# Kernel tuning notes

Measured on AMD Instinct MI355X. Metric: run time of the kernel, lower is better.

## Reference

```python
import jax, jax.numpy as jnp
import numpy as np

N, E, F, H, L, G = 100000, 1600000, 32, 128, 4, 64


def gru_cell(m, h, w_ih, b_ih, w_hh, b_hh):
    # torch.nn.GRUCell math; gate order: r, z, n
    gi = m @ w_ih.T + b_ih          # [N, 3H]
    gh = h @ w_hh.T + b_hh          # [N, 3H]
    i_r, i_z, i_n = jnp.split(gi, 3, axis=-1)
    h_r, h_z, h_n = jnp.split(gh, 3, axis=-1)
    r = jax.nn.sigmoid(i_r + h_r)
    z = jax.nn.sigmoid(i_z + h_z)
    n = jnp.tanh(i_n + r * h_n)
    return (1.0 - z) * n + z * h


def setup_inputs() -> dict:
    key = jax.random.key(0)
    ks = jax.random.split(key, 12)
    s = 0.05
    return {
        "x": jax.random.normal(ks[0], (N, F), jnp.float32),
        "edge_index": jax.random.randint(ks[1], (2, E), 0, N, jnp.int64),
        "batch": jnp.sort(jax.random.randint(ks[2], (N,), 0, G, jnp.int64)),
        "num_graphs": G,
        "W0": jax.random.normal(ks[3], (H, F), jnp.float32) * s,
        "conv_w": jax.random.normal(ks[4], (L, H, H), jnp.float32) * s,
        "w_ih": jax.random.normal(ks[5], (3 * H, H), jnp.float32) * s,
        "b_ih": jax.random.normal(ks[6], (3 * H,), jnp.float32) * s,
        "w_hh": jax.random.normal(ks[7], (3 * H, H), jnp.float32) * s,
        "b_hh": jax.random.normal(ks[8], (3 * H,), jnp.float32) * s,
        "lin1_w": jax.random.normal(ks[9], (1, H), jnp.float32) * s,
        "lin1_b": jax.random.normal(ks[10], (1,), jnp.float32) * s,
    }


def reference(x, edge_index, batch, num_graphs, W0, conv_w, w_ih, b_ih, w_hh, b_hh, lin1_w, lin1_b):
    n_nodes = x.shape[0]
    # lin0 (no bias) + sigmoid embedding
    x_embed = jax.nn.sigmoid(x @ W0.T)                     # [N, H]

    src, dst = edge_index[0], edge_index[1]
    h = x_embed
    # GatedGraphConv: per layer, transform -> scatter-add over edges -> GRU update
    for l in range(conv_w.shape[0]):
        m = h @ conv_w[l]                                   # [N, H]
        agg = jax.ops.segment_sum(m[src], dst, num_segments=n_nodes)  # [N, H]
        h = gru_cell(agg, h, w_ih, b_ih, w_hh, b_hh)

    h = jax.nn.relu(h)
    out = h @ lin1_w.T + lin1_b                             # [N, 1]
    uncorrected = out

    # per-graph mean subtraction (scatter_mean + gather), same math as the loop
    sums = jax.ops.segment_sum(out, batch, num_segments=num_graphs)   # [G, 1]
    counts = jax.ops.segment_sum(jnp.ones((n_nodes, 1), out.dtype), batch, num_segments=num_graphs)
    mean_all = sums / jnp.maximum(counts, 1.0)
    corrected = out - mean_all[batch]

    return corrected.squeeze(1), x_embed, uncorrected.squeeze(1)
```

## Files before the change

### kernel.cpp

```cpp
#include <hip/hip_runtime.h>
#include <hip/hip_bf16.h>

#define HDIM 128
#define FDIM 32
#define GGR  64
#define SCAN_CHUNK 2048
#define FILL_CHUNK 1024
#define FILL_WIN 16

typedef __attribute__((ext_vector_type(8))) short bf16x8;
typedef __attribute__((ext_vector_type(4))) float f32x4;

__device__ __forceinline__ float fsig(float x) {
  return __builtin_amdgcn_rcpf(1.f + __expf(-x));
}
__device__ __forceinline__ float ftanh(float x) {
  return 1.f - 2.f * __builtin_amdgcn_rcpf(1.f + __expf(2.f * x));
}

__device__ __forceinline__ bf16x8 pack_bf16x8(float4 a, float4 b) {
  union { bf16x8 v; __hip_bfloat162 h[4]; } u;
  u.h[0] = __float22bfloat162_rn(make_float2(a.x, a.y));
  u.h[1] = __float22bfloat162_rn(make_float2(a.z, a.w));
  u.h[2] = __float22bfloat162_rn(make_float2(b.x, b.y));
  u.h[3] = __float22bfloat162_rn(make_float2(b.z, b.w));
  return u.v;
}

__device__ __forceinline__ int ablk(int kb, int m) {
  return (kb << 6) + (m & 56) + ((m ^ kb) & 7);
}

__device__ __forceinline__ void stage64(const unsigned short* __restrict__ g,
                                        short* __restrict__ s, int n0, int N, int t) {
#pragma unroll
  for (int r = 0; r < 2; ++r) {
    int idx = r * 512 + t;
    int m = idx >> 4, c8 = idx & 15;
    int gn = n0 + m;
    uint4 v = make_uint4(0u, 0u, 0u, 0u);
    if (gn < N) v = *(const uint4*)(g + (size_t)gn * HDIM + c8 * 8);
    *(uint4*)(s + ablk(c8, m) * 8) = v;
  }
}


__global__ __launch_bounds__(256) void k_embed_hist(const float* __restrict__ x,
                                                    const unsigned short* __restrict__ W0b,
                                                    unsigned short* __restrict__ hb,
                                                    float* __restrict__ xemb,
                                                    int N,
                                                    const int* __restrict__ dst,
                                                    int* __restrict__ deg,
                                                    unsigned short* __restrict__ rank,
                                                    long long E, int histBlocks, int q8) {
  if ((int)blockIdx.x < histBlocks) {
    long long e = (long long)blockIdx.x * 256 + threadIdx.x;
    if (e < E) {
      int old = atomicAdd(&deg[dst[e]], 1);
      rank[e] = (unsigned short)old;
    }
    return;
  }
  int p = blockIdx.x - histBlocks;
  int T = (p & 7) * q8 + (p >> 3);
  int n0 = T * 64;
  if (n0 >= N) return;
  int t = threadIdx.x;
  int w = t >> 6, l = t & 63;
  int lm = l & 15, lq = l >> 4;
  int j0 = w * 32;
  bf16x8 b0 = *(const bf16x8*)(W0b + (size_t)(j0 + lm) * FDIM + lq * 8);
  bf16x8 b1 = *(const bf16x8*)(W0b + (size_t)(j0 + 16 + lm) * FDIM + lq * 8);
  f32x4 acc0[4], acc1[4];
#pragma unroll
  for (int i = 0; i < 4; ++i) { acc0[i] = (f32x4){0.f,0.f,0.f,0.f}; acc1[i] = (f32x4){0.f,0.f,0.f,0.f}; }
#pragma unroll
  for (int tt = 0; tt < 4; ++tt) {
    int rg = n0 + tt * 16 + lm;
    bf16x8 a = (bf16x8){0,0,0,0,0,0,0,0};
    if (rg < N) {
      const float4* xr = (const float4*)x + (size_t)rg * 8 + lq * 2;
      a = pack_bf16x8(xr[0], xr[1]);
    }
    acc0[tt] = __builtin_amdgcn_mfma_f32_16x16x32_bf16(a, b0, acc0[tt], 0, 0, 0);
    acc1[tt] = __builtin_amdgcn_mfma_f32_16x16x32_bf16(a, b1, acc1[tt], 0, 0, 0);
  }
#pragma unroll
  for (int g = 0; g < 2; ++g) {
    int j = j0 + g * 16 + lm;
#pragma unroll
    for (int tt = 0; tt < 4; ++tt)
#pragma unroll
      for (int r = 0; r < 4; ++r) {
        int node = n0 + tt * 16 + lq * 4 + r;
        if (node < N) {
          float v = g ? acc1[tt][r] : acc0[tt][r];
          float e = fsig(v);
          size_t off = (size_t)node * HDIM + j;
          xemb[off] = e;
          ((__hip_bfloat16*)hb)[off] = __float2bfloat16(e);
        }
      }
  }
}

__global__ __launch_bounds__(256) void k_prep_w(const float* __restrict__ w_ih,
                                                const float* __restrict__ w_hh,
                                                const float* __restrict__ conv_w,
                                                const float* __restrict__ W0,
                                                unsigned short* __restrict__ wIb,
                                                unsigned short* __restrict__ wHb,
                                                unsigned short* __restrict__ convTb,
                                                unsigned short* __restrict__ W0b,
                                                int L) {
  int i = blockIdx.x * 256 + threadIdx.x;
  if (i < HDIM * FDIM) ((__hip_bfloat16*)W0b)[i] = __float2bfloat16(W0[i]);
  if (i < 384 * HDIM) {
    ((__hip_bfloat16*)wIb)[i] = __float2bfloat16(w_ih[i]);
    ((__hip_bfloat16*)wHb)[i] = __float2bfloat16(w_hh[i]);
  }
  int total = L * HDIM * HDIM;
  if (i < total) {
    int l = i >> 14, rem = i & 16383, j = rem >> 7, k = rem & 127;
    ((__hip_bfloat16*)convTb)[i] = __float2bfloat16(conv_w[(l << 14) + (k << 7) + j]);
  }
}

__global__ __launch_bounds__(256) void k_block_sum(const int* __restrict__ deg,
                                                   int* __restrict__ bsum, int N) {
  int base = blockIdx.x * SCAN_CHUNK + threadIdx.x * 8;
  int s = 0;
#pragma unroll
  for (int u = 0; u < 8; ++u) { int i = base + u; if (i < N) s += deg[i]; }
#pragma unroll
  for (int o = 32; o; o >>= 1) s += __shfl_down(s, o, 64);
  __shared__ int wsum[4];
  if ((threadIdx.x & 63) == 0) wsum[threadIdx.x >> 6] = s;
  __syncthreads();
  if (threadIdx.x == 0) bsum[blockIdx.x] = wsum[0] + wsum[1] + wsum[2] + wsum[3];
}

__global__ void k_scan_bsums(int* __restrict__ bsum, int nb) {
  if (blockIdx.x == 0 && threadIdx.x == 0) {
    int run = 0;
    for (int i = 0; i < nb; ++i) { int v = bsum[i]; bsum[i] = run; run += v; }
  }
}

__global__ __launch_bounds__(256) void k_scan_chunks(const int* __restrict__ deg,
                                                     const int* __restrict__ bsum,
                                                     int* __restrict__ rowstart,
                                                     int N, int Etot) {
  __shared__ int ts[256];
  int base = blockIdx.x * SCAN_CHUNK + threadIdx.x * 8;
  int loc[8]; int s = 0;
#pragma unroll
  for (int u = 0; u < 8; ++u) {
    int i = base + u; loc[u] = s;
    s += (i < N) ? deg[i] : 0;
  }
  ts[threadIdx.x] = s;
  __syncthreads();
  for (int o = 1; o < 256; o <<= 1) {
    int v = (threadIdx.x >= o) ? ts[threadIdx.x - o] : 0;
    __syncthreads();
    ts[threadIdx.x] += v;
    __syncthreads();
  }
  int texcl = (threadIdx.x ? ts[threadIdx.x - 1] : 0) + bsum[blockIdx.x];
#pragma unroll
  for (int u = 0; u < 8; ++u) {
    int i = base + u;
    if (i < N) rowstart[i] = texcl + loc[u];
  }
  if (blockIdx.x == 0 && threadIdx.x == 0) rowstart[N] = Etot;
}

__global__ __launch_bounds__(256) void k_csr_fill_win(const int* __restrict__ src,
                                                      const int* __restrict__ dst,
                                                      const unsigned short* __restrict__ rank,
                                                      const int* __restrict__ rowstart,
                                                      int* __restrict__ csr,
                                                      long long E, int N) {
  __shared__ int sd[FILL_CHUNK];
  __shared__ int ss[FILL_CHUNK];
  __shared__ unsigned short sr[FILL_CHUNK];
  long long base = (long long)blockIdx.x * FILL_CHUNK;
  int cnt = (int)((E - base < FILL_CHUNK) ? (E - base) : FILL_CHUNK);
  for (int i = threadIdx.x; i < cnt; i += 256) {
    sd[i] = dst[base + i];
    ss[i] = src[base + i];
    sr[i] = rank[base + i];
  }
  __syncthreads();
  int nw = (N + FILL_WIN - 1) / FILL_WIN;
#pragma unroll 1
  for (int w = 0; w < FILL_WIN; ++w) {
    int lo = w * nw, hi = lo + nw;
    for (int i = threadIdx.x; i < cnt; i += 256) {
      int d = sd[i];
      if (d >= lo && d < hi)
        csr[rowstart[d] + sr[i]] = ss[i];
    }
    __syncthreads();
  }
}

__global__ __launch_bounds__(256) void k_gather(const int* __restrict__ csr,
                                                const int* __restrict__ rowstart,
                                                const unsigned short* __restrict__ m,
                                                unsigned short* __restrict__ agg, int N, int q8) {
  int p = blockIdx.x;
  int G = (p & 7) * q8 * 16 + (p >> 3);
  int wv = threadIdx.x >> 6, l = threadIdx.x & 63;
  int n = G * 4 + wv;
  if (n >= N) return;
  int eq = l >> 3;
  int jb = l & 7;
  int beg = rowstart[n], end = rowstart[n + 1];
  float acc[16];
#pragma unroll
  for (int i = 0; i < 16; ++i) acc[i] = 0.f;
  for (int e0 = beg; e0 < end; e0 += 8) {
    int e = e0 + eq;
    uint4 v0 = make_uint4(0u, 0u, 0u, 0u);
    uint4 v1 = make_uint4(0u, 0u, 0u, 0u);
    if (e < end) {
      int s = csr[e];
      const uint4* row = (const uint4*)(m + (size_t)s * HDIM + jb * 16);
      v0 = row[0];
      v1 = row[1];
    }
    acc[0]  += __uint_as_float(v0.x << 16);
    acc[1]  += __uint_as_float(v0.x & 0xffff0000u);
    acc[2]  += __uint_as_float(v0.y << 16);
    acc[3]  += __uint_as_float(v0.y & 0xffff0000u);
    acc[4]  += __uint_as_float(v0.z << 16);
    acc[5]  += __uint_as_float(v0.z & 0xffff0000u);
    acc[6]  += __uint_as_float(v0.w << 16);
    acc[7]  += __uint_as_float(v0.w & 0xffff0000u);
    acc[8]  += __uint_as_float(v1.x << 16);
    acc[9]  += __uint_as_float(v1.x & 0xffff0000u);
    acc[10] += __uint_as_float(v1.y << 16);
    acc[11] += __uint_as_float(v1.y & 0xffff0000u);
    acc[12] += __uint_as_float(v1.z << 16);
    acc[13] += __uint_as_float(v1.z & 0xffff0000u);
    acc[14] += __uint_as_float(v1.w << 16);
    acc[15] += __uint_as_float(v1.w & 0xffff0000u);
  }
#pragma unroll
  for (int i = 0; i < 16; ++i) {
    acc[i] += __shfl_xor(acc[i], 8, 64);
    acc[i] += __shfl_xor(acc[i], 16, 64);
    acc[i] += __shfl_xor(acc[i], 32, 64);
  }
  if (eq == 0) {
    union { uint4 v[2]; __hip_bfloat162 h[8]; } o;
#pragma unroll
    for (int i = 0; i < 8; ++i)
      o.h[i] = __float22bfloat162_rn(make_float2(acc[2 * i], acc[2 * i + 1]));
    uint4* dstp = (uint4*)(agg + (size_t)n * HDIM + jb * 16);
    dstp[0] = o.v[0];
    dstp[1] = o.v[1];
  }
}

__global__ __launch_bounds__(512, 4) void k_gru_mfma(const unsigned short* __restrict__ hsum,
                                                  const unsigned short* __restrict__ hb,
                                                  const unsigned short* __restrict__ wT,
                                                  const unsigned short* __restrict__ wI,
                                                  const unsigned short* __restrict__ wH,
                                                  const float* __restrict__ b_ih,
                                                  const float* __restrict__ b_hh,
                                                  unsigned short* __restrict__ hnewb,
                                                  int N, int q8) {
  __shared__ short sAg[16 * 64 * 8];
  __shared__ short sH[16 * 64 * 8];
  int p = blockIdx.x;
  int T = (p & 7) * q8 + (p >> 3);
  int n0 = T * 64;
  if (n0 >= N) return;
  int t = threadIdx.x;
  stage64(hsum, sAg, n0, N, t);
  stage64(hb, sH, n0, N, t);
  int w = t >> 6, l = t & 63;
  int j0 = w * 16;
  int lm = l & 15, lq = l >> 4;
  int j = j0 + lm;
  float bir = b_ih[j], biz = b_ih[j + 128], bin = b_ih[j + 256];
  float bhr = b_hh[j], bhz = b_hh[j + 128], bhn = b_hh[j + 256];
  __syncthreads();
  {
    f32x4 macc[4];
#pragma unroll
    for (int i = 0; i < 4; ++i) macc[i] = (f32x4){0.f,0.f,0.f,0.f};
#pragma unroll
    for (int ks = 0; ks < 4; ++ks) {
      bf16x8 b = *(const bf16x8*)(wT + (size_t)(j0 + lm) * HDIM + ks * 32 + lq * 8);
      int kb = ks * 4 + lq;
#pragma unroll
      for (int tt = 0; tt < 4; ++tt) {
        bf16x8 a = *(const bf16x8*)(sAg + ablk(kb, tt * 16 + lm) * 8);
        macc[tt] = __builtin_amdgcn_mfma_f32_16x16x32_bf16(a, b, macc[tt], 0, 0, 0);
      }
    }
    __syncthreads();
#pragma unroll
    for (int tt = 0; tt < 4; ++tt)
#pragma unroll
      for (int r = 0; r < 4; ++r) {
        int m = tt * 16 + lq * 4 + r;
        ((__hip_bfloat16*)sAg)[ablk(j >> 3, m) * 8 + (j & 7)] = __float2bfloat16(macc[tt][r]);
      }
  }
  __syncthreads();
  f32x4 aR[4], aZ[4], aNi[4], aNh[4];
#pragma unroll
  for (int i = 0; i < 4; ++i) {
    aR[i] = (f32x4){0.f,0.f,0.f,0.f}; aZ[i] = (f32x4){0.f,0.f,0.f,0.f};
    aNi[i] = (f32x4){0.f,0.f,0.f,0.f}; aNh[i] = (f32x4){0.f,0.f,0.f,0.f};
  }
#pragma unroll
  for (int ks = 0; ks < 4; ++ks) {
    size_t rI = (size_t)(j0 + lm) * HDIM + ks * 32 + lq * 8;
    bf16x8 bIr = *(const bf16x8*)(wI + rI);
    bf16x8 bIz = *(const bf16x8*)(wI + rI + 128 * HDIM);
    bf16x8 bIn = *(const bf16x8*)(wI + rI + 256 * HDIM);
    bf16x8 bHr = *(const bf16x8*)(wH + rI);
    bf16x8 bHz = *(const bf16x8*)(wH + rI + 128 * HDIM);
    bf16x8 bHn = *(const bf16x8*)(wH + rI + 256 * HDIM);
    int kb = ks * 4 + lq;
#pragma unroll
    for (int tt = 0; tt < 4; ++tt) {
      bf16x8 a = *(const bf16x8*)(sAg + ablk(kb, tt * 16 + lm) * 8);
      bf16x8 h = *(const bf16x8*)(sH + ablk(kb, tt * 16 + lm) * 8);
      aR[tt] = __builtin_amdgcn_mfma_f32_16x16x32_bf16(a, bIr, aR[tt], 0, 0, 0);
      aR[tt] = __builtin_amdgcn_mfma_f32_16x16x32_bf16(h, bHr, aR[tt], 0, 0, 0);
      aZ[tt] = __builtin_amdgcn_mfma_f32_16x16x32_bf16(a, bIz, aZ[tt], 0, 0, 0);
      aZ[tt] = __builtin_amdgcn_mfma_f32_16x16x32_bf16(h, bHz, aZ[tt], 0, 0, 0);
      aNi[tt] = __builtin_amdgcn_mfma_f32_16x16x32_bf16(a, bIn, aNi[tt], 0, 0, 0);
      aNh[tt] = __builtin_amdgcn_mfma_f32_16x16x32_bf16(h, bHn, aNh[tt], 0, 0, 0);
    }
  }
#pragma unroll
  for (int tt = 0; tt < 4; ++tt)
#pragma unroll
    for (int r = 0; r < 4; ++r) {
      int m = tt * 16 + lq * 4 + r;
      int node = n0 + m;
      float hp = __bfloat162float(((const __hip_bfloat16*)sH)[ablk(j >> 3, m) * 8 + (j & 7)]);
      float rg = fsig(aR[tt][r] + bir + bhr);
      float zg = fsig(aZ[tt][r] + biz + bhz);
      float nv = aNi[tt][r] + bin + rg * (aNh[tt][r] + bhn);
      float th = ftanh(nv);
      float hn = (1.f - zg) * th + zg * hp;
      if (node < N)
        ((__hip_bfloat16*)hnewb)[(size_t)node * HDIM + j] = __float2bfloat16(hn);
    }
}

__global__ __launch_bounds__(512, 4) void k_gru_last(const unsigned short* __restrict__ hsum,
                                                  const unsigned short* __restrict__ hb,
                                                  const unsigned short* __restrict__ wT,
                                                  const unsigned short* __restrict__ wI,
                                                  const unsigned short* __restrict__ wH,
                                                  const float* __restrict__ b_ih,
                                                  const float* __restrict__ b_hh,
                                                  const float* __restrict__ w1,
                                                  const float* __restrict__ b1,
                                                  float* __restrict__ out_raw,
                                                  float* __restrict__ out_unc,
                                                  int N, int q8) {
  __shared__ short sAg[16 * 64 * 8];
  __shared__ short sH[16 * 64 * 8];
  __shared__ float sOut[64];
  int p = blockIdx.x;
  int T = (p & 7) * q8 + (p >> 3);
  int n0 = T * 64;
  if (n0 >= N) return;
  int t = threadIdx.x;
  stage64(hsum, sAg, n0, N, t);
  stage64(hb, sH, n0, N, t);
  if (t < 64) sOut[t] = 0.f;
  int w = t >> 6, l = t & 63;
  int j0 = w * 16;
  int lm = l & 15, lq = l >> 4;
  int j = j0 + lm;
  float bir = b_ih[j], biz = b_ih[j + 128], bin = b_ih[j + 256];
  float bhr = b_hh[j], bhz = b_hh[j + 128], bhn = b_hh[j + 256];
  float w1j = w1[j];
  __syncthreads();
  {
    f32x4 macc[4];
#pragma unroll
    for (int i = 0; i < 4; ++i) macc[i] = (f32x4){0.f,0.f,0.f,0.f};
#pragma unroll
    for (int ks = 0; ks < 4; ++ks) {
      bf16x8 b = *(const bf16x8*)(wT + (size_t)(j0 + lm) * HDIM + ks * 32 + lq * 8);
      int kb = ks * 4 + lq;
#pragma unroll
      for (int tt = 0; tt < 4; ++tt) {
        bf16x8 a = *(const bf16x8*)(sAg + ablk(kb, tt * 16 + lm) * 8);
        macc[tt] = __builtin_amdgcn_mfma_f32_16x16x32_bf16(a, b, macc[tt], 0, 0, 0);
      }
    }
    __syncthreads();
#pragma unroll
    for (int tt = 0; tt < 4; ++tt)
#pragma unroll
      for (int r = 0; r < 4; ++r) {
        int m = tt * 16 + lq * 4 + r;
        ((__hip_bfloat16*)sAg)[ablk(j >> 3, m) * 8 + (j & 7)] = __float2bfloat16(macc[tt][r]);
      }
  }
  __syncthreads();
  f32x4 aR[4], aZ[4], aNi[4], aNh[4];
#pragma unroll
  for (int i = 0; i < 4; ++i) {
    aR[i] = (f32x4){0.f,0.f,0.f,0.f}; aZ[i] = (f32x4){0.f,0.f,0.f,0.f};
    aNi[i] = (f32x4){0.f,0.f,0.f,0.f}; aNh[i] = (f32x4){0.f,0.f,0.f,0.f};
  }
#pragma unroll
  for (int ks = 0; ks < 4; ++ks) {
    size_t rI = (size_t)(j0 + lm) * HDIM + ks * 32 + lq * 8;
    bf16x8 bIr = *(const bf16x8*)(wI + rI);
    bf16x8 bIz = *(const bf16x8*)(wI + rI + 128 * HDIM);
    bf16x8 bIn = *(const bf16x8*)(wI + rI + 256 * HDIM);
    bf16x8 bHr = *(const bf16x8*)(wH + rI);
    bf16x8 bHz = *(const bf16x8*)(wH + rI + 128 * HDIM);
    bf16x8 bHn = *(const bf16x8*)(wH + rI + 256 * HDIM);
    int kb = ks * 4 + lq;
#pragma unroll
    for (int tt = 0; tt < 4; ++tt) {
      bf16x8 a = *(const bf16x8*)(sAg + ablk(kb, tt * 16 + lm) * 8);
      bf16x8 h = *(const bf16x8*)(sH + ablk(kb, tt * 16 + lm) * 8);
      aR[tt] = __builtin_amdgcn_mfma_f32_16x16x32_bf16(a, bIr, aR[tt], 0, 0, 0);
      aR[tt] = __builtin_amdgcn_mfma_f32_16x16x32_bf16(h, bHr, aR[tt], 0, 0, 0);
      aZ[tt] = __builtin_amdgcn_mfma_f32_16x16x32_bf16(a, bIz, aZ[tt], 0, 0, 0);
      aZ[tt] = __builtin_amdgcn_mfma_f32_16x16x32_bf16(h, bHz, aZ[tt], 0, 0, 0);
      aNi[tt] = __builtin_amdgcn_mfma_f32_16x16x32_bf16(a, bIn, aNi[tt], 0, 0, 0);
      aNh[tt] = __builtin_amdgcn_mfma_f32_16x16x32_bf16(h, bHn, aNh[tt], 0, 0, 0);
    }
  }
  __syncthreads();
#pragma unroll
  for (int tt = 0; tt < 4; ++tt)
#pragma unroll
    for (int r = 0; r < 4; ++r) {
      int m = tt * 16 + lq * 4 + r;
      int node = n0 + m;
      float hp = __bfloat162float(((const __hip_bfloat16*)sH)[ablk(j >> 3, m) * 8 + (j & 7)]);
      float rg = fsig(aR[tt][r] + bir + bhr);
      float zg = fsig(aZ[tt][r] + biz + bhz);
      float nv = aNi[tt][r] + bin + rg * (aNh[tt][r] + bhn);
      float th = ftanh(nv);
      float hn = (1.f - zg) * th + zg * hp;
      float prt = (node < N) ? fmaxf(hn, 0.f) * w1j : 0.f;
      prt += __shfl_xor(prt, 1, 64);
      prt += __shfl_xor(prt, 2, 64);
      prt += __shfl_xor(prt, 4, 64);
      prt += __shfl_xor(prt, 8, 64);
      if (lm == 0) atomicAdd(&sOut[m], prt);
    }
  __syncthreads();
  if (t < 64) {
    int node = n0 + t;
    if (node < N) {
      float o = sOut[t] + b1[0];
      out_raw[node] = o;
      out_unc[node] = o;
    }
  }
}

__global__ __launch_bounds__(256) void k_graph_reduce(const float* __restrict__ out_raw,
                                                      const int* __restrict__ batch,
                                                      float* __restrict__ gsum,
                                                      float* __restrict__ gcnt,
                                                      int N) {
  __shared__ float ls[GGR], lc[GGR];
  int t = threadIdx.x;
  if (t < GGR) { ls[t] = 0.f; lc[t] = 0.f; }
  __syncthreads();
  for (int n = blockIdx.x * 256 + t; n < N; n += gridDim.x * 256) {
    int g = batch[n];
    atomicAdd(&ls[g], out_raw[n]);
    atomicAdd(&lc[g], 1.f);
  }
  __syncthreads();
  if (t < GGR) {
    unsafeAtomicAdd(&gsum[t], ls[t]);
    unsafeAtomicAdd(&gcnt[t], lc[t]);
  }
}

__global__ __launch_bounds__(256) void k_correct(const float* __restrict__ out_raw,
                                                 const int* __restrict__ batch,
                                                 const float* __restrict__ gsum,
                                                 const float* __restrict__ gcnt,
                                                 float* __restrict__ corrected, int N) {
  int n = blockIdx.x * 256 + threadIdx.x;
  if (n < N) {
    int g = batch[n];
    corrected[n] = out_raw[n] - gsum[g] / fmaxf(gcnt[g], 1.f);
  }
}

extern "C" void kernel_launch(void* const* d_in, const int* in_sizes, int n_in,
                              void* d_out, int out_size, void* d_ws, size_t ws_size,
                              hipStream_t stream) {
  const float* x      = (const float*)d_in[0];
  const int*   ei     = (const int*)d_in[1];
  const int*   batch  = (const int*)d_in[2];
  const float* W0     = (const float*)d_in[4];
  const float* conv_w = (const float*)d_in[5];
  const float* w_ih   = (const float*)d_in[6];
  const float* b_ih   = (const float*)d_in[7];
  const float* w_hh   = (const float*)d_in[8];
  const float* b_hh   = (const float*)d_in[9];
  const float* lin1_w = (const float*)d_in[10];
  const float* lin1_b = (const float*)d_in[11];

  int N = in_sizes[0] / FDIM;
  long long E = in_sizes[1] / 2;
  int L = in_sizes[5] / (HDIM * HDIM);

  const int* src = ei;
  const int* dstv = ei + E;

  float* out_corrected = (float*)d_out;
  float* out_xemb = out_corrected + N;
  float* out_unc  = out_xemb + (size_t)N * HDIM;

  char* p = (char*)d_ws;
  unsigned short* x0 = (unsigned short*)p; p += (size_t)N * HDIM * 2;
  unsigned short* x1 = (unsigned short*)p; p += (size_t)N * HDIM * 2;
  unsigned short* x2 = (unsigned short*)p; p += (size_t)N * HDIM * 2;
  float* out_raw = (float*)p;        p += (size_t)((N + 3) & ~3) * 4;
  float* gsum = (float*)p;           p += GGR * 4;
  float* gcnt = (float*)p;           p += GGR * 4;
  int* deg = (int*)p;                p += (size_t)((N + 3) & ~3) * 4;
  int* rowstart = (int*)p;           p += (size_t)(N + 4) * 4;
  int nb = (N + SCAN_CHUNK - 1) / SCAN_CHUNK;
  int* bsum = (int*)p;               p += (size_t)((nb + 63) & ~63) * 4;
  int* csr = (int*)p;                p += (size_t)E * 4;
  unsigned short* rankb = (unsigned short*)p;  p += (size_t)((E + 3) & ~3) * 2;
  unsigned short* wIb = (unsigned short*)p;    p += 384 * HDIM * 2;
  unsigned short* wHb = (unsigned short*)p;    p += 384 * HDIM * 2;
  unsigned short* convTb = (unsigned short*)p; p += (size_t)L * HDIM * HDIM * 2;
  unsigned short* W0b = (unsigned short*)p;

  int prep_total = (384 * HDIM > L * HDIM * HDIM) ? 384 * HDIM : L * HDIM * HDIM;
  k_prep_w<<<(prep_total + 255) / 256, 256, 0, stream>>>(w_ih, w_hh, conv_w, W0, wIb, wHb, convTb, W0b, L);

  hipMemsetAsync(deg, 0, (size_t)N * sizeof(int), stream);
  hipMemsetAsync(gsum, 0, 2 * GGR * sizeof(float), stream);

  int nblk = (N + 63) / 64;
  int TP = (nblk + 7) & ~7;
  int q8 = TP / 8;
  int histBlocks = (int)((E + 255) / 256);
  k_embed_hist<<<histBlocks + TP, 256, 0, stream>>>(x, W0b, x0, out_xemb, N,
                                                    dstv, deg, rankb, E, histBlocks, q8);

  k_block_sum<<<nb, 256, 0, stream>>>(deg, bsum, N);
  k_scan_bsums<<<1, 64, 0, stream>>>(bsum, nb);
  k_scan_chunks<<<nb, 256, 0, stream>>>(deg, bsum, rowstart, N, (int)E);
  k_csr_fill_win<<<(int)((E + FILL_CHUNK - 1) / FILL_CHUNK), 256, 0, stream>>>(
      src, dstv, rankb, rowstart, csr, E, N);

  unsigned short* Hb = x0;
  unsigned short* Fb = x1;
  for (int l = 0; l < L; ++l) {
    k_gather<<<TP * 16, 256, 0, stream>>>(csr, rowstart, Hb, x2, N, q8);
    const unsigned short* wTl = convTb + (size_t)l * HDIM * HDIM;
    if (l + 1 < L) {
      k_gru_mfma<<<TP, 512, 0, stream>>>(x2, Hb, wTl, wIb, wHb, b_ih, b_hh, Fb, N, q8);
      unsigned short* tmp = Hb; Hb = Fb; Fb = tmp;
    } else {
      k_gru_last<<<TP, 512, 0, stream>>>(x2, Hb, wTl, wIb, wHb, b_ih, b_hh,
                                         lin1_w, lin1_b, out_raw, out_unc, N, q8);
    }
  }

  k_graph_reduce<<<256, 256, 0, stream>>>(out_raw, batch, gsum, gcnt, N);
  k_correct<<<(N + 255) / 256, 256, 0, stream>>>(out_raw, batch, gsum, gcnt, out_corrected, N);
}
```

Measured before the change: 715.5 us.

## Split embedding tiles between histogram and CSR fill kernels for overlap

```diff
diff --git a/kernel.cpp b/kernel.cpp
--- a/kernel.cpp
+++ b/kernel.cpp
@@ -44,26 +44,11 @@
   }
 }
 
-
-__global__ __launch_bounds__(256) void k_embed_hist(const float* __restrict__ x,
-                                                    const unsigned short* __restrict__ W0b,
-                                                    unsigned short* __restrict__ hb,
-                                                    float* __restrict__ xemb,
-                                                    int N,
-                                                    const int* __restrict__ dst,
-                                                    int* __restrict__ deg,
-                                                    unsigned short* __restrict__ rank,
-                                                    long long E, int histBlocks, int q8) {
-  if ((int)blockIdx.x < histBlocks) {
-    long long e = (long long)blockIdx.x * 256 + threadIdx.x;
-    if (e < E) {
-      int old = atomicAdd(&deg[dst[e]], 1);
-      rank[e] = (unsigned short)old;
-    }
-    return;
-  }
-  int p = blockIdx.x - histBlocks;
-  int T = (p & 7) * q8 + (p >> 3);
+__device__ __forceinline__ void embed_tile(const float* __restrict__ x,
+                                           const unsigned short* __restrict__ W0b,
+                                           unsigned short* __restrict__ hb,
+                                           float* __restrict__ xemb,
+                                           int N, int T) {
   int n0 = T * 64;
   if (n0 >= N) return;
   int t = threadIdx.x;
@@ -103,6 +88,81 @@
         }
       }
   }
+}
+
+
+__global__ __launch_bounds__(256) void k_embed_hist(const float* __restrict__ x,
+                                                    const unsigned short* __restrict__ W0b,
+                                                    unsigned short* __restrict__ hb,
+                                                    float* __restrict__ xemb,
+                                                    int N,
+                                                    const int* __restrict__ dst,
+                                                    int* __restrict__ deg,
+                                                    unsigned short* __restrict__ rank,
+                                                    long long E, int histBlocks, int q8,
+                                                    int tileCnt) {
+  if ((int)blockIdx.x < histBlocks) {
+    long long e = (long long)blockIdx.x * 256 + threadIdx.x;
+    if (e < E) {
+      int old = atomicAdd(&deg[dst[e]], 1);
+      rank[e] = (unsigned short)old;
+    }
+    return;
+  }
+  int idx = blockIdx.x - histBlocks;
+  if (idx >= tileCnt) return;
+  int T = (idx & 7) * q8 + (idx >> 3);
+  embed_tile(x, W0b, hb, xemb, N, T);
+}
+
+__global__ __launch_bounds__(256) void k_embed_fill(const float* __restrict__ x,
+                                                    const unsigned short* __restrict__ W0b,
+                                                    unsigned short* __restrict__ hb,
+                                                    float* __restrict__ xemb,
+                                                    int N,
+                                                    const int* __restrict__ src,
+                                                    const int* __restrict__ dst,
+                                                    const unsigned short* __restrict__ rank,
+                                                    const int* __restrict__ rowstart,
+                                                    int* __restrict__ csr,
+                                                    long long E, int FB, int q8,
+                                                    int tileOff, int tileCnt) {
+  __shared__ int sd[FILL_CHUNK];
+  __shared__ int ss[FILL_CHUNK];
+  __shared__ unsigned short sr[FILL_CHUNK];
+  int p = blockIdx.x;
+  int M2 = ((tileCnt < FB) ? tileCnt : FB) * 2;
+  bool isFill; int idx;
+  if (p < M2) { isFill = (p & 1); idx = p >> 1; }
+  else { idx = p - (M2 >> 1); isFill = (FB > tileCnt); }
+
+  if (isFill) {
+    if (idx >= FB) return;
+    long long base = (long long)idx * FILL_CHUNK;
+    int cnt = (int)((E - base < FILL_CHUNK) ? (E - base) : FILL_CHUNK);
+    for (int i = threadIdx.x; i < cnt; i += 256) {
+      sd[i] = dst[base + i];
+      ss[i] = src[base + i];
+      sr[i] = rank[base + i];
+    }
+    __syncthreads();
+    int nw = (N + FILL_WIN - 1) / FILL_WIN;
+#pragma unroll 1
+    for (int w = 0; w < FILL_WIN; ++w) {
+      int lo = w * nw, hi = lo + nw;
+      for (int i = threadIdx.x; i < cnt; i += 256) {
+        int d = sd[i];
+        if (d >= lo && d < hi)
+          csr[rowstart[d] + sr[i]] = ss[i];
+      }
+      __syncthreads();
+    }
+    return;
+  }
+  if (idx >= tileCnt) return;
+  int gidx = tileOff + idx;
+  int T = (gidx & 7) * q8 + (gidx >> 3);
+  embed_tile(x, W0b, hb, xemb, N, T);
 }
 
 __global__ __launch_bounds__(256) void k_prep_w(const float* __restrict__ w_ih,
@@ -175,36 +235,6 @@
     if (i < N) rowstart[i] = texcl + loc[u];
   }
   if (blockIdx.x == 0 && threadIdx.x == 0) rowstart[N] = Etot;
-}
-
-__global__ __launch_bounds__(256) void k_csr_fill_win(const int* __restrict__ src,
-                                                      const int* __restrict__ dst,
-                                                      const unsigned short* __restrict__ rank,
-                                                      const int* __restrict__ rowstart,
-                                                      int* __restrict__ csr,
-                                                      long long E, int N) {
-  __shared__ int sd[FILL_CHUNK];
-  __shared__ int ss[FILL_CHUNK];
-  __shared__ unsigned short sr[FILL_CHUNK];
-  long long base = (long long)blockIdx.x * FILL_CHUNK;
-  int cnt = (int)((E - base < FILL_CHUNK) ? (E - base) : FILL_CHUNK);
-  for (int i = threadIdx.x; i < cnt; i += 256) {
-    sd[i] = dst[base + i];
-    ss[i] = src[base + i];
-    sr[i] = rank[base + i];
-  }
-  __syncthreads();
-  int nw = (N + FILL_WIN - 1) / FILL_WIN;
-#pragma unroll 1
-  for (int w = 0; w < FILL_WIN; ++w) {
-    int lo = w * nw, hi = lo + nw;
-    for (int i = threadIdx.x; i < cnt; i += 256) {
-      int d = sd[i];
-      if (d >= lo && d < hi)
-        csr[rowstart[d] + sr[i]] = ss[i];
-    }
-    __syncthreads();
-  }
 }
 
 __global__ __launch_bounds__(256) void k_gather(const int* __restrict__ csr,
@@ -561,14 +591,17 @@
   int TP = (nblk + 7) & ~7;
   int q8 = TP / 8;
   int histBlocks = (int)((E + 255) / 256);
-  k_embed_hist<<<histBlocks + TP, 256, 0, stream>>>(x, W0b, x0, out_xemb, N,
-                                                    dstv, deg, rankb, E, histBlocks, q8);
-
+  int FB = (int)((E + FILL_CHUNK - 1) / FILL_CHUNK);
+  int TA = TP / 2;
+  int TB = TP - TA;
+
+  k_embed_hist<<<histBlocks + TA, 256, 0, stream>>>(x, W0b, x0, out_xemb, N,
+                                                    dstv, deg, rankb, E, histBlocks, q8, TA);
   k_block_sum<<<nb, 256, 0, stream>>>(deg, bsum, N);
   k_scan_bsums<<<1, 64, 0, stream>>>(bsum, nb);
   k_scan_chunks<<<nb, 256, 0, stream>>>(deg, bsum, rowstart, N, (int)E);
-  k_csr_fill_win<<<(int)((E + FILL_CHUNK - 1) / FILL_CHUNK), 256, 0, stream>>>(
-      src, dstv, rankb, rowstart, csr, E, N);
+  k_embed_fill<<<TB + FB, 256, 0, stream>>>(x, W0b, x0, out_xemb, N,
+                                            src, dstv, rankb, rowstart, csr, E, FB, q8, TA, TB);
 
   unsigned short* Hb = x0;
   unsigned short* Fb = x1;
```

Result: no change. 722.1 us (+0.9%).
